# Performance work log

Hardware: AMD Instinct MI355X
Metric: run time of the kernel (lower is better)

## Reference

```python
import jax, jax.numpy as jnp
import numpy as np
import math

# Model dims (see shape_source)
N_EMBD = 2048
QK_H = 128      # per-head qk dim
V_H = 128       # per-head v dim
Q_DIM = N_EMBD                 # 2048 -> 16 query heads
N_HEAD = Q_DIM // QK_H         # 16
KV_HEAD = N_HEAD // 4          # 4 (GQA)
K_DIM = KV_HEAD * QK_H         # 512
V_DIM = KV_HEAD * V_H          # 512
D_KV = K_DIM + V_DIM           # 1024, S6 channel dim
D_STATE = 16                   # S6 state size
DT_RANK = math.ceil(D_KV / 16) # 'auto' -> 64
WINDOW = 512
B, T = 1, 4096


def setup_inputs() -> dict:
    key = jax.random.key(0)
    ks = jax.random.split(key, 8)
    x = jax.random.normal(ks[0], (B, T, N_EMBD), jnp.float32)
    W_attn = jax.random.normal(ks[1], (Q_DIM + K_DIM + V_DIM, N_EMBD), jnp.float32) * 0.02
    # S6 params (canonical Mamba S6 init: A = -exp(A_log), A_log = log(1..N))
    A_log = jnp.log(jnp.arange(1, D_STATE + 1, dtype=jnp.float32))[None, :] * jnp.ones((D_KV, 1), jnp.float32)
    x_proj_w = jax.random.normal(ks[2], (DT_RANK + 2 * D_STATE, D_KV), jnp.float32) * 0.02
    dt_proj_w = jax.random.normal(ks[3], (D_KV, DT_RANK), jnp.float32) * 0.02
    dt_proj_b = jax.random.normal(ks[4], (D_KV,), jnp.float32) * 0.1
    D_param = jnp.ones((D_KV,), jnp.float32)
    W_o = jax.random.normal(ks[5], (N_EMBD, Q_DIM), jnp.float32) * 0.02
    return dict(x=x, W_attn=W_attn, A_log=A_log, x_proj_w=x_proj_w,
                dt_proj_w=dt_proj_w, dt_proj_b=dt_proj_b, D_param=D_param,
                W_o=W_o, window_size=WINDOW)


def s6_scan(u, A_log, x_proj_w, dt_proj_w, dt_proj_b, D_param):
    """Canonical S6 selective scan. u: (B, T, D) -> (B, T, D)."""
    Bb, Tt, D = u.shape
    N = A_log.shape[1]
    dt_rank = dt_proj_w.shape[1]
    x_dbl = jnp.einsum('btd,ed->bte', u, x_proj_w)          # (B,T,dt_rank+2N)
    dt, Bm, Cm = jnp.split(x_dbl, [dt_rank, dt_rank + N], axis=-1)
    delta = jax.nn.softplus(jnp.einsum('btr,dr->btd', dt, dt_proj_w) + dt_proj_b)  # (B,T,D)
    A = -jnp.exp(A_log)                                      # (D,N), negative
    dA = jnp.exp(delta[..., None] * A)                       # (B,T,D,N)
    dBu = delta[..., None] * Bm[:, :, None, :] * u[..., None]  # (B,T,D,N)

    def step(h, inp):
        dA_t, dBu_t, C_t = inp
        h = dA_t * h + dBu_t                                 # (B,D,N)
        y = jnp.einsum('bdn,bn->bd', h, C_t)
        return h, y

    h0 = jnp.zeros((Bb, D, N), u.dtype)
    _, ys = jax.lax.scan(step, h0,
                         (dA.transpose(1, 0, 2, 3), dBu.transpose(1, 0, 2, 3), Cm.transpose(1, 0, 2)))
    y = ys.transpose(1, 0, 2)                                # (B,T,D)
    return y + D_param * u


def sliding_window_attn(q, k, v, window, scale):
    """Causal sliding-window attention; query i attends to j in [i-(window-1), i].
    q: (B,T,H,dh), k/v: (B,T,Hk,dh). Blockwise with one look-back block."""
    Bb, Tt, H, dh = q.shape
    Hk = k.shape[2]
    G = H // Hk
    k = jnp.repeat(k, G, axis=2)
    v = jnp.repeat(v, G, axis=2)
    W = window
    nb = Tt // W
    # (B,H,nb,W,dh)
    qb = q.reshape(Bb, nb, W, H, dh).transpose(0, 3, 1, 2, 4)
    kb = k.reshape(Bb, nb, W, H, dh).transpose(0, 3, 1, 2, 4)
    vb = v.reshape(Bb, nb, W, H, dh).transpose(0, 3, 1, 2, 4)
    # previous block (zeros for first block)
    kprev = jnp.pad(kb, ((0, 0), (0, 0), (1, 0), (0, 0), (0, 0)))[:, :, :nb]
    vprev = jnp.pad(vb, ((0, 0), (0, 0), (1, 0), (0, 0), (0, 0)))[:, :, :nb]
    k2 = jnp.concatenate([kprev, kb], axis=3)                # (B,H,nb,2W,dh)
    v2 = jnp.concatenate([vprev, vb], axis=3)
    scores = jnp.einsum('bhwid,bhwjd->bhwij', qb * scale, k2)  # (B,H,nb,W,2W)
    i = jnp.arange(W)[:, None]
    j = jnp.arange(2 * W)[None, :]
    rel = i + W - j                                          # absolute i - j
    base_mask = (rel >= 0) & (rel <= W - 1)                  # causal & within window
    blk = jnp.arange(nb)[:, None, None]
    valid = base_mask[None] & ((j[None] >= W) | (blk > 0))   # first block: no look-back
    neg = jnp.finfo(jnp.float32).max
    scores = jnp.where(valid[None, None], scores, -neg)
    attn = jax.nn.softmax(scores.astype(jnp.float32), axis=-1).astype(q.dtype)
    out = jnp.einsum('bhwij,bhwjd->bhwid', attn, v2)         # (B,H,nb,W,dh)
    return out.transpose(0, 2, 3, 1, 4).reshape(Bb, Tt, H, dh)


def reference(x, W_attn, A_log, x_proj_w, dt_proj_w, dt_proj_b, D_param, W_o, window_size):
    Bb, Tt, C = x.shape
    qkv = jnp.einsum('btc,oc->bto', x, W_attn)
    q = qkv[..., :Q_DIM]
    kv = qkv[..., Q_DIM:]
    kv = s6_scan(kv, A_log, x_proj_w, dt_proj_w, dt_proj_b, D_param)
    k = kv[..., :K_DIM]
    v = kv[..., K_DIM:]
    q = q.reshape(Bb, Tt, N_HEAD, QK_H)
    k = k.reshape(Bb, Tt, KV_HEAD, QK_H)
    v = v.reshape(Bb, Tt, KV_HEAD, V_H)
    scale = 1.0 / math.sqrt(QK_H)
    y = sliding_window_attn(q, k, v, window_size, scale)     # (B,T,H,v_h)
    y = y.reshape(Bb, Tt, -1)
    return jnp.einsum('bto,no->btn', y, W_o)
```

## Files before the change

kernel.cpp:

```cpp
#include <hip/hip_runtime.h>
#include <hip/hip_bf16.h>

typedef __hip_bfloat16 bf16;
typedef __attribute__((ext_vector_type(8))) short bf16x8;
typedef __attribute__((ext_vector_type(4))) float f32x4;

#define T_SEQ 4096
#define NEMBD 2048
#define QKVD  3072
#define QDIM  2048
#define DKV   1024
#define KDIM  512
#define NH    16
#define DH    128
#define NST   16
#define DTR   64
#define WIN   512
#define NCHUNK 64
#define CLEN   64

__device__ inline float bf2f(bf16 x) { return __bfloat162float(x); }

struct F8 { float v[8]; };

__device__ inline F8 load_b8(const bf16* p) {
  union { uint4 q; unsigned short s[8]; } u;
  u.q = *reinterpret_cast<const uint4*>(p);
  F8 r;
#pragma unroll
  for (int i = 0; i < 8; i++) r.v[i] = __uint_as_float((unsigned)u.s[i] << 16);
  return r;
}

__device__ inline F8 load8(const void* base, size_t idx, int f32flag) {
  if (f32flag) {
    const float4* p = reinterpret_cast<const float4*>((const float*)base + idx);
    float4 a = p[0], b = p[1];
    F8 r;
    r.v[0]=a.x; r.v[1]=a.y; r.v[2]=a.z; r.v[3]=a.w;
    r.v[4]=b.x; r.v[5]=b.y; r.v[6]=b.z; r.v[7]=b.w;
    return r;
  }
  return load_b8((const bf16*)base + idx);
}

__device__ inline float load1(const void* base, size_t idx, int f32flag) {
  return f32flag ? ((const float*)base)[idx] : bf2f(((const bf16*)base)[idx]);
}

__device__ inline unsigned short f2b_bits(float f) {
  bf16 h = __float2bfloat16(f);
  union { bf16 h; unsigned short u; } c; c.h = h; return c.u;
}

__device__ inline ushort4 pack4(float a, float b, float c, float d) {
  ushort4 r; r.x = f2b_bits(a); r.y = f2b_bits(b); r.z = f2b_bits(c); r.w = f2b_bits(d);
  return r;
}

__device__ inline void gld_lds16(const void* g, void* l) {
  __builtin_amdgcn_global_load_lds(
      (const __attribute__((address_space(1))) unsigned int*)g,
      (__attribute__((address_space(3))) unsigned int*)l, 16, 0, 0);
}

__global__ void detect_dtype(const unsigned short* __restrict__ x, int* __restrict__ flag) {
  if (threadIdx.x == 0 && blockIdx.x == 0) {
    int c = 0;
    for (int i = 0; i < 128; i++) {
      float v = __uint_as_float((unsigned)x[i] << 16);
      float a = fabsf(v);
      if (a >= 1e-8f && a <= 1e4f) c++;
    }
    flag[0] = (c >= 120) ? 0 : 1;
  }
}

__global__ __launch_bounds__(256) void cvt_bf16(
    const void* __restrict__ in, const int* __restrict__ dflag,
    unsigned short* __restrict__ out, int n8)
{
  int i = blockIdx.x * 256 + threadIdx.x;
  if (i >= n8) return;
  const int f = dflag[0];
  F8 v = load8(in, (size_t)i * 8, f);
  ushort4* o = (ushort4*)(out + (size_t)i * 8);
  o[0] = pack4(v.v[0], v.v[1], v.v[2], v.v[3]);
  o[1] = pack4(v.v[4], v.v[5], v.v[6], v.v[7]);
}

__global__ __launch_bounds__(512, 2) void gemm_wide(
    const unsigned short* __restrict__ A, const unsigned short* __restrict__ B,
    int M, int N, int K, int mode,
    bf16* __restrict__ oq, bf16* __restrict__ ou, float* __restrict__ oc)
{
  __shared__ unsigned short lds[2][384 * 64];
  const int tid = threadIdx.x;
  const int wave = tid >> 6, lane = tid & 63;
  const int quad = lane >> 4, l16 = lane & 15;
  const int wm = wave >> 1, wn = wave & 1;
  const int nbx = N >> 7;
  const int nwg = gridDim.x;
  const int chunk = nwg >> 3;
  const int swz = (blockIdx.x & 7) * chunk + (blockIdx.x >> 3);
  const int bm = (swz / nbx) * 256, bn = (swz % nbx) * 128;

  const int lrow = lane >> 3;
  const int lslot = (lane & 7) ^ lrow;
  const unsigned short* Abase = A + (size_t)(bm + wave * 8 + lrow) * K + lslot * 8;
  const unsigned short* Bbase = B + (size_t)(bn + wave * 8 + lrow) * K + lslot * 8;

  const int x7 = l16 & 7;
  const int s0 = ((0 + quad) ^ x7) * 8;
  const int s1 = ((4 + quad) ^ x7) * 8;
  const int arow0 = (wm * 64 + l16) * 64;
  const int brow0 = (256 + wn * 64 + l16) * 64;

  f32x4 acc[4][4];
#pragma unroll
  for (int i = 0; i < 4; i++)
#pragma unroll
    for (int j = 0; j < 4; j++) acc[i][j] = f32x4{0.f, 0.f, 0.f, 0.f};

  const int NT = K >> 6;

#pragma unroll
  for (int grp = 0; grp < 4; grp++)
    gld_lds16(Abase + (size_t)grp * 64 * K, &lds[0][(grp * 64 + wave * 8) * 64]);
#pragma unroll
  for (int grp = 0; grp < 2; grp++)
    gld_lds16(Bbase + (size_t)grp * 64 * K, &lds[0][(256 + grp * 64 + wave * 8) * 64]);
#pragma unroll
  for (int grp = 0; grp < 4; grp++)
    gld_lds16(Abase + (size_t)grp * 64 * K + 64, &lds[1][(grp * 64 + wave * 8) * 64]);
#pragma unroll
  for (int grp = 0; grp < 2; grp++)
    gld_lds16(Bbase + (size_t)grp * 64 * K + 64, &lds[1][(256 + grp * 64 + wave * 8) * 64]);
  asm volatile("s_waitcnt vmcnt(6)" ::: "memory");
  __builtin_amdgcn_sched_barrier(0);
  __builtin_amdgcn_s_barrier();

#define MM(m, n) \
  acc[m][n] = __builtin_amdgcn_mfma_f32_16x16x32_bf16(aF[m][0], bF[n][0], acc[m][n], 0, 0, 0); \
  acc[m][n] = __builtin_amdgcn_mfma_f32_16x16x32_bf16(aF[m][1], bF[n][1], acc[m][n], 0, 0, 0);

  for (int g = 0; g < NT; ++g) {
    const unsigned short* L = lds[g & 1];
    unsigned short* Lw = (unsigned short*)L;
    const bool stF = (g + 2) < NT;
    const size_t kF = (size_t)(g + 2) * 64;

    bf16x8 aF[4][2], bF[4][2];

#pragma unroll
    for (int m = 0; m < 4; m++) {
      aF[m][0] = *(const bf16x8*)&L[arow0 + m * 1024 + s0];
      aF[m][1] = *(const bf16x8*)&L[arow0 + m * 1024 + s1];
    }
    bF[0][0] = *(const bf16x8*)&L[brow0 +    0 + s0];
    bF[0][1] = *(const bf16x8*)&L[brow0 +    0 + s1];
    bF[1][0] = *(const bf16x8*)&L[brow0 + 1024 + s0];
    bF[1][1] = *(const bf16x8*)&L[brow0 + 1024 + s1];
    __builtin_amdgcn_s_barrier();
    if (stF) {
#pragma unroll
      for (int grp = 0; grp < 4; grp++)
        gld_lds16(Abase + (size_t)grp * 64 * K + kF, &Lw[(grp * 64 + wave * 8) * 64]);
    }
    __builtin_amdgcn_s_setprio(1);
    MM(0,0); MM(0,1); MM(1,0); MM(1,1);
    MM(2,0); MM(2,1); MM(3,0); MM(3,1);
    __builtin_amdgcn_s_setprio(0);
    __builtin_amdgcn_s_barrier();

    bF[2][0] = *(const bf16x8*)&L[brow0 + 2048 + s0];
    bF[2][1] = *(const bf16x8*)&L[brow0 + 2048 + s1];
    bF[3][0] = *(const bf16x8*)&L[brow0 + 3072 + s0];
    bF[3][1] = *(const bf16x8*)&L[brow0 + 3072 + s1];
    __builtin_amdgcn_s_barrier();
    if (stF) {
#pragma unroll
      for (int grp = 0; grp < 2; grp++)
        gld_lds16(Bbase + (size_t)grp * 64 * K + kF, &Lw[(256 + grp * 64 + wave * 8) * 64]);
    }
    __builtin_amdgcn_s_setprio(1);
    MM(0,2); MM(0,3); MM(1,2); MM(1,3);
    MM(2,2); MM(2,3); MM(3,2); MM(3,3);
    __builtin_amdgcn_s_setprio(0);
    if (stF) { asm volatile("s_waitcnt vmcnt(6)" ::: "memory"); }
    else     { asm volatile("s_waitcnt vmcnt(0)" ::: "memory"); }
    __builtin_amdgcn_sched_barrier(0);
    __builtin_amdgcn_s_barrier();
  }
#undef MM

#pragma unroll
  for (int m = 0; m < 4; m++)
#pragma unroll
    for (int n = 0; n < 4; n++) {
      int gm0 = bm + wm * 64 + m * 16 + quad * 4;
      int gn  = bn + wn * 64 + n * 16 + l16;
#pragma unroll
      for (int r = 0; r < 4; r++) {
        int gm = gm0 + r;
        float v = acc[m][n][r];
        if (mode == 0) {
          if (gn < QDIM) oq[(size_t)gm * QDIM + gn] = __float2bfloat16(v);
          else           ou[(size_t)gm * DKV + (gn - QDIM)] = __float2bfloat16(v);
        } else {
          oc[(size_t)gm * N + gn] = v;
        }
      }
    }
}

__global__ __launch_bounds__(256) void xdbl_mfma(
    const bf16* __restrict__ u, const unsigned short* __restrict__ xpw_bf,
    float* __restrict__ xd)
{
  __shared__ unsigned short Us[64 * 32];
  __shared__ unsigned short Ws[96 * 32];
  const int tid = threadIdx.x;
  const int wave = tid >> 6, lane = tid & 63;
  const int quad = lane >> 4, l16 = lane & 15;
  const int t0 = blockIdx.x * 64;
  const unsigned short* ub = (const unsigned short*)u;

  f32x4 acc[6];
#pragma unroll
  for (int j = 0; j < 6; j++) acc[j] = f32x4{0.f, 0.f, 0.f, 0.f};

  const int urow = tid >> 2, ucol = (tid & 3) * 8;
  const int wrow0 = tid >> 2, wcol0 = (tid & 3) * 8;
  const int wrow1 = (256 + tid) >> 2;

  uint4 upre = *(const uint4*)(ub + (size_t)(t0 + urow) * DKV + ucol);
  uint4 wpre0 = *(const uint4*)(xpw_bf + (size_t)wrow0 * DKV + wcol0);
  uint4 wpre1 = (tid < 128) ? *(const uint4*)(xpw_bf + (size_t)wrow1 * DKV + wcol0)
                            : uint4{0, 0, 0, 0};

  for (int k0 = 0; k0 < DKV; k0 += 32) {
    __syncthreads();
    *(uint4*)&Us[urow * 32 + ucol] = upre;
    *(uint4*)&Ws[wrow0 * 32 + wcol0] = wpre0;
    if (tid < 128) *(uint4*)&Ws[wrow1 * 32 + wcol0] = wpre1;
    __syncthreads();

    int kn = (k0 + 32 < DKV) ? (k0 + 32) : k0;
    upre  = *(const uint4*)(ub + (size_t)(t0 + urow) * DKV + kn + ucol);
    wpre0 = *(const uint4*)(xpw_bf + (size_t)wrow0 * DKV + kn + wcol0);
    if (tid < 128) wpre1 = *(const uint4*)(xpw_bf + (size_t)wrow1 * DKV + kn + wcol0);

    bf16x8 a = *(const bf16x8*)&Us[(wave * 16 + l16) * 32 + quad * 8];
#pragma unroll
    for (int j = 0; j < 6; j++) {
      bf16x8 b = *(const bf16x8*)&Ws[(j * 16 + l16) * 32 + quad * 8];
      acc[j] = __builtin_amdgcn_mfma_f32_16x16x32_bf16(a, b, acc[j], 0, 0, 0);
    }
  }

#pragma unroll
  for (int j = 0; j < 6; j++)
#pragma unroll
    for (int r = 0; r < 4; r++) {
      int t = t0 + wave * 16 + quad * 4 + r;
      xd[(size_t)t * 96 + j * 16 + l16] = acc[j][r];
    }
}

__global__ __launch_bounds__(256) void delta_mfma(
    const float* __restrict__ xd, const unsigned short* __restrict__ dtw_bf,
    const void* __restrict__ dtb, const int* __restrict__ dflag,
    bf16* __restrict__ delta)
{
  __shared__ unsigned short Xs[64 * 72];
  __shared__ unsigned short Ws[128 * 72];
  const int tid = threadIdx.x;
  const int wave = tid >> 6, lane = tid & 63;
  const int quad = lane >> 4, l16 = lane & 15;
  const int t0 = blockIdx.y * 64, d0 = blockIdx.x * 128;

  for (int e = tid; e < 64 * 8; e += 256) {
    int row = e >> 3, c8 = (e & 7) * 8;
    const float* p = xd + (size_t)(t0 + row) * 96 + c8;
    float4 a = *(const float4*)p, b = *(const float4*)(p + 4);
    *(ushort4*)&Xs[row * 72 + c8]     = pack4(a.x, a.y, a.z, a.w);
    *(ushort4*)&Xs[row * 72 + c8 + 4] = pack4(b.x, b.y, b.z, b.w);
  }
  for (int e = tid; e < 128 * 8; e += 256) {
    int row = e >> 3, c8 = (e & 7) * 8;
    *(uint4*)&Ws[row * 72 + c8] = *(const uint4*)(dtw_bf + (size_t)(d0 + row) * DTR + c8);
  }
  __syncthreads();

  bf16x8 a0 = *(const bf16x8*)&Xs[(wave * 16 + l16) * 72 + quad * 8];
  bf16x8 a1 = *(const bf16x8*)&Xs[(wave * 16 + l16) * 72 + 32 + quad * 8];

  f32x4 acc[8];
#pragma unroll
  for (int j = 0; j < 8; j++) {
    bf16x8 b0 = *(const bf16x8*)&Ws[(j * 16 + l16) * 72 + quad * 8];
    bf16x8 b1 = *(const bf16x8*)&Ws[(j * 16 + l16) * 72 + 32 + quad * 8];
    acc[j] = __builtin_amdgcn_mfma_f32_16x16x32_bf16(a0, b0, f32x4{0.f, 0.f, 0.f, 0.f}, 0, 0, 0);
    acc[j] = __builtin_amdgcn_mfma_f32_16x16x32_bf16(a1, b1, acc[j], 0, 0, 0);
  }

  const int f = dflag[0];
#pragma unroll
  for (int j = 0; j < 8; j++) {
    int d = d0 + j * 16 + l16;
    float bias = load1(dtb, d, f);
#pragma unroll
    for (int r = 0; r < 4; r++) {
      int t = t0 + wave * 16 + quad * 4 + r;
      float v = acc[j][r] + bias;
      float sp = fmaxf(v, 0.f) + log1pf(expf(-fabsf(v)));
      delta[(size_t)t * DKV + d] = __float2bfloat16(sp);
    }
  }
}

__global__ __launch_bounds__(256) void scan_pass1(
    const bf16* __restrict__ delta, const bf16* __restrict__ u,
    const float* __restrict__ xd, const void* __restrict__ A_log,
    const int* __restrict__ dflag, float* __restrict__ Pb, float* __restrict__ Hl)
{
  const int gid = blockIdx.x * 256 + threadIdx.x;
  const int c = gid >> 14;
  const int r = gid & 16383;
  const int d = r >> 4, n = r & 15;
  const int f = dflag[0];
  const float A = -expf(load1(A_log, d * NST + n, f));
  float p = 1.f, h = 0.f;
  const int t0 = c * CLEN;
  for (int tt = 0; tt < CLEN; tt++) {
    int t = t0 + tt;
    float dl = bf2f(delta[(size_t)t * DKV + d]);
    float uu = bf2f(u[(size_t)t * DKV + d]);
    float bm = xd[(size_t)t * 96 + DTR + n];
    float a = expf(dl * A);
    h = a * h + dl * bm * uu;
    p *= a;
  }
  Pb[gid] = p;
  Hl[gid] = h;
}

__global__ __launch_bounds__(256) void scan_combine(
    float* __restrict__ Pb, const float* __restrict__ Hl)
{
  const int idx = blockIdx.x * 256 + threadIdx.x;
  float run = 0.f;
  for (int c = 0; c < NCHUNK; c++) {
    size_t off = (size_t)c * 16384 + idx;
    float p = Pb[off], hl = Hl[off];
    Pb[off] = run;
    run = p * run + hl;
  }
}

__global__ __launch_bounds__(256) void scan_pass2(
    const bf16* __restrict__ delta, bf16* __restrict__ u,
    const float* __restrict__ xd, const void* __restrict__ A_log,
    const void* __restrict__ Dp, const int* __restrict__ dflag,
    const float* __restrict__ Hin)
{
  const int gid = blockIdx.x * 256 + threadIdx.x;
  const int c = gid >> 14;
  const int r = gid & 16383;
  const int d = r >> 4, n = r & 15;
  const int f = dflag[0];
  const float A = -expf(load1(A_log, d * NST + n, f));
  const float dpar = load1(Dp, d, f);
  float h = Hin[gid];
  const int t0 = c * CLEN;
  for (int tt = 0; tt < CLEN; tt++) {
    int t = t0 + tt;
    float dl = bf2f(delta[(size_t)t * DKV + d]);
    float uu = bf2f(u[(size_t)t * DKV + d]);
    float bm = xd[(size_t)t * 96 + DTR + n];
    float cm = xd[(size_t)t * 96 + DTR + NST + n];
    float a = expf(dl * A);
    h = a * h + dl * bm * uu;
    float part = h * cm;
    part += __shfl_xor(part, 1);
    part += __shfl_xor(part, 2);
    part += __shfl_xor(part, 4);
    part += __shfl_xor(part, 8);
    if (n == 0) u[(size_t)t * DKV + d] = __float2bfloat16(part + dpar * uu);
  }
}

__global__ __launch_bounds__(256) void vtrans(
    const bf16* __restrict__ kv, unsigned short* __restrict__ vt)
{
  __shared__ float tile[64][68];
  const int tt0 = blockIdx.x * 64, d0 = blockIdx.y * 64;
  const int tid = threadIdx.x;
  for (int e = tid; e < 64 * 8; e += 256) {
    int row = e >> 3, c8 = (e & 7) * 8;
    F8 v = load_b8(kv + (size_t)(tt0 + row) * DKV + KDIM + d0 + c8);
#pragma unroll
    for (int j = 0; j < 8; j++) tile[row][c8 + j] = v.v[j];
  }
  __syncthreads();
  for (int e = tid; e < 64 * 8; e += 256) {
    int dd = e >> 3, t8 = (e & 7) * 8;
    float vv[8];
#pragma unroll
    for (int j = 0; j < 8; j++) vv[j] = tile[t8 + j][dd];
    ushort4* o = (ushort4*)(vt + (size_t)(d0 + dd) * T_SEQ + tt0 + t8);
    o[0] = pack4(vv[0], vv[1], vv[2], vv[3]);
    o[1] = pack4(vv[4], vv[5], vv[6], vv[7]);
  }
}

__global__ __launch_bounds__(256, 4) void attn_mfma(
    const bf16* __restrict__ q, const bf16* __restrict__ kv,
    const unsigned short* __restrict__ vt, bf16* __restrict__ y)
{
  __shared__ unsigned short Ks[32 * 136];
  __shared__ unsigned short Vts[128 * 40];
  __shared__ unsigned short Ps[4][16 * 40];
  const int tid = threadIdx.x;
  const int wave = tid >> 6, lane = tid & 63;
  const int quad = lane >> 4, l16 = lane & 15;
  const int qt = blockIdx.x, h = blockIdx.y, kvh = h >> 2;
  const int t0 = qt * 64;
  const float scale = 0.088388347648318447f;

  bf16x8 af[4];
#pragma unroll
  for (int s = 0; s < 4; s++)
    af[s] = *(const bf16x8*)(q + (size_t)(t0 + wave * 16 + l16) * QDIM
                             + h * DH + s * 32 + quad * 8);

  const int krow = tid >> 4, kc8 = (tid & 15) * 8;
  const int vrow = tid >> 2, vc8 = (tid & 3) * 8;
  const bf16* kgp = kv + (size_t)kvh * DH;
  const unsigned short* vgp = vt + (size_t)(kvh * DH) * T_SEQ;

  float m_r[4], l_p[4];
  f32x4 O[8];
#pragma unroll
  for (int r = 0; r < 4; r++) { m_r[r] = -1e30f; l_p[r] = 0.f; }
#pragma unroll
  for (int dt = 0; dt < 8; dt++) O[dt] = f32x4{0.f, 0.f, 0.f, 0.f};

  const int kb_start = (t0 > WIN - 1) ? ((t0 - (WIN - 1)) >> 5) : 0;
  const int kb_end = (t0 + 63) >> 5;

  uint4 kp0, kp1, vp0, vp1;
  {
    const int kb = kb_start;
    kp0 = *(const uint4*)(kgp + (size_t)(kb * 32 + krow) * DKV + kc8);
    kp1 = *(const uint4*)(kgp + (size_t)(kb * 32 + 16 + krow) * DKV + kc8);
    vp0 = *(const uint4*)(vgp + (size_t)vrow * T_SEQ + kb * 32 + vc8);
    vp1 = *(const uint4*)(vgp + (size_t)(vrow + 64) * T_SEQ + kb * 32 + vc8);
  }

  for (int kb = kb_start; kb <= kb_end; kb++) {
    __syncthreads();
    *(uint4*)&Ks[krow * 136 + kc8]        = kp0;
    *(uint4*)&Ks[(krow + 16) * 136 + kc8] = kp1;
    *(uint4*)&Vts[vrow * 40 + vc8]        = vp0;
    *(uint4*)&Vts[(vrow + 64) * 40 + vc8] = vp1;
    __syncthreads();

    if (kb < kb_end) {
      const int kn = kb + 1;
      kp0 = *(const uint4*)(kgp + (size_t)(kn * 32 + krow) * DKV + kc8);
      kp1 = *(const uint4*)(kgp + (size_t)(kn * 32 + 16 + krow) * DKV + kc8);
      vp0 = *(const uint4*)(vgp + (size_t)vrow * T_SEQ + kn * 32 + vc8);
      vp1 = *(const uint4*)(vgp + (size_t)(vrow + 64) * T_SEQ + kn * 32 + vc8);
    }

    f32x4 S0 = f32x4{0.f, 0.f, 0.f, 0.f}, S1 = f32x4{0.f, 0.f, 0.f, 0.f};
#pragma unroll
    for (int s = 0; s < 4; s++) {
      bf16x8 b0 = *(const bf16x8*)&Ks[(l16) * 136 + s * 32 + quad * 8];
      bf16x8 b1 = *(const bf16x8*)&Ks[(16 + l16) * 136 + s * 32 + quad * 8];
      S0 = __builtin_amdgcn_mfma_f32_16x16x32_bf16(af[s], b0, S0, 0, 0, 0);
      S1 = __builtin_amdgcn_mfma_f32_16x16x32_bf16(af[s], b1, S1, 0, 0, 0);
    }

    const int ka0 = kb * 32 + l16;
    const int ka1 = ka0 + 16;
    const bool full = (kb * 32 >= t0 + 63 - (WIN - 1)) && (kb * 32 + 31 <= t0);

    float v0r[4], v1r[4];
    bool x0r[4], x1r[4];
    bool ok = true;
#pragma unroll
    for (int r = 0; r < 4; r++) {
      int qa = t0 + wave * 16 + quad * 4 + r;
      float v0 = S0[r] * scale, v1 = S1[r] * scale;
      bool x0 = true, x1 = true;
      if (!full) {
        x0 = (ka0 <= qa) && (ka0 > qa - WIN);
        x1 = (ka1 <= qa) && (ka1 > qa - WIN);
        if (!x0) v0 = -1e30f;
        if (!x1) v1 = -1e30f;
      }
      v0r[r] = v0; v1r[r] = v1; x0r[r] = x0; x1r[r] = x1;
      ok = ok && (fmaxf(v0, v1) <= m_r[r] + 8.f);
    }

    if (!__all((int)ok)) {
#pragma unroll
      for (int r = 0; r < 4; r++) {
        float rm = fmaxf(v0r[r], v1r[r]);
        rm = fmaxf(rm, __shfl_xor(rm, 1));
        rm = fmaxf(rm, __shfl_xor(rm, 2));
        rm = fmaxf(rm, __shfl_xor(rm, 4));
        rm = fmaxf(rm, __shfl_xor(rm, 8));
        float mnew = fmaxf(m_r[r], rm);
        float al = __expf(m_r[r] - mnew);
        m_r[r] = mnew;
        l_p[r] *= al;
#pragma unroll
        for (int dt = 0; dt < 8; dt++) O[dt][r] *= al;
      }
    }

#pragma unroll
    for (int r = 0; r < 4; r++) {
      float p0 = x0r[r] ? __expf(v0r[r] - m_r[r]) : 0.f;
      float p1 = x1r[r] ? __expf(v1r[r] - m_r[r]) : 0.f;
      l_p[r] += p0 + p1;
      Ps[wave][(quad * 4 + r) * 40 + l16]      = f2b_bits(p0);
      Ps[wave][(quad * 4 + r) * 40 + 16 + l16] = f2b_bits(p1);
    }

    bf16x8 pa = *(const bf16x8*)&Ps[wave][l16 * 40 + quad * 8];
#pragma unroll
    for (int dt = 0; dt < 8; dt++) {
      bf16x8 b = *(const bf16x8*)&Vts[(dt * 16 + l16) * 40 + quad * 8];
      O[dt] = __builtin_amdgcn_mfma_f32_16x16x32_bf16(pa, b, O[dt], 0, 0, 0);
    }
  }

  float inv[4];
#pragma unroll
  for (int r = 0; r < 4; r++) {
    float l = l_p[r];
    l += __shfl_xor(l, 1);
    l += __shfl_xor(l, 2);
    l += __shfl_xor(l, 4);
    l += __shfl_xor(l, 8);
    inv[r] = 1.f / l;
  }
#pragma unroll
  for (int dt = 0; dt < 8; dt++)
#pragma unroll
    for (int r = 0; r < 4; r++) {
      int row = t0 + wave * 16 + quad * 4 + r;
      y[(size_t)row * QDIM + h * DH + dt * 16 + l16] = __float2bfloat16(O[dt][r] * inv[r]);
    }
}

extern "C" void kernel_launch(void* const* d_in, const int* in_sizes, int n_in,
                              void* d_out, int out_size, void* d_ws, size_t ws_size,
                              hipStream_t stream)
{
  const void* x      = d_in[0];
  const void* W_attn = d_in[1];
  const void* A_log  = d_in[2];
  const void* xpw    = d_in[3];
  const void* dtw    = d_in[4];
  const void* dtb    = d_in[5];
  const void* Dp     = d_in[6];
  const void* W_o    = d_in[7];

  char* ws = (char*)d_ws;
  int*   dflag = (int*)ws;   ws += 256;
  bf16*  u     = (bf16*)ws;  ws += (size_t)T_SEQ * DKV * 2;
  float* xd    = (float*)ws; ws += (size_t)T_SEQ * 96 * 4;
  char*  yreg  = ws;
  bf16*  delta = (bf16*)ws;  ws += (size_t)T_SEQ * DKV * 2;
  float* Pb    = (float*)ws; ws += (size_t)NCHUNK * DKV * NST * 4;
  float* Hl    = (float*)ws; ws += (size_t)NCHUNK * DKV * NST * 4;
  unsigned short* x_bf  = (unsigned short*)ws; ws += (size_t)T_SEQ * NEMBD * 2;
  unsigned short* wa_bf = (unsigned short*)ws; ws += (size_t)QKVD * NEMBD * 2;
  unsigned short* wo_bf = (unsigned short*)ws; ws += (size_t)NEMBD * QDIM * 2;
  unsigned short* vt    = (unsigned short*)ws; ws += (size_t)KDIM * T_SEQ * 2;
  unsigned short* xpw_bf = (unsigned short*)ws; ws += (size_t)96 * DKV * 2;
  unsigned short* dtw_bf = (unsigned short*)ws; ws += (size_t)DKV * DTR * 2;
  bf16*  y     = (bf16*)yreg;

  bf16*  q_bf = (bf16*)d_out;
  float* out  = (float*)d_out;

  detect_dtype<<<1, 64, 0, stream>>>((const unsigned short*)x, dflag);
  cvt_bf16<<<(T_SEQ * NEMBD / 8 + 255) / 256, 256, 0, stream>>>(x, dflag, x_bf, T_SEQ * NEMBD / 8);
  cvt_bf16<<<(QKVD * NEMBD / 8 + 255) / 256, 256, 0, stream>>>(W_attn, dflag, wa_bf, QKVD * NEMBD / 8);
  cvt_bf16<<<(NEMBD * QDIM / 8 + 255) / 256, 256, 0, stream>>>(W_o, dflag, wo_bf, NEMBD * QDIM / 8);
  cvt_bf16<<<(96 * DKV / 8 + 255) / 256, 256, 0, stream>>>(xpw, dflag, xpw_bf, 96 * DKV / 8);
  cvt_bf16<<<(DKV * DTR / 8 + 255) / 256, 256, 0, stream>>>(dtw, dflag, dtw_bf, DKV * DTR / 8);

  gemm_wide<<<(T_SEQ / 256) * (QKVD / 128), 512, 0, stream>>>(
      x_bf, wa_bf, T_SEQ, QKVD, NEMBD, 0, q_bf, u, nullptr);
  xdbl_mfma<<<T_SEQ / 64, 256, 0, stream>>>(u, xpw_bf, xd);
  delta_mfma<<<dim3(DKV / 128, T_SEQ / 64), 256, 0, stream>>>(xd, dtw_bf, dtb, dflag, delta);
  scan_pass1<<<4096, 256, 0, stream>>>(delta, u, xd, A_log, dflag, Pb, Hl);
  scan_combine<<<64, 256, 0, stream>>>(Pb, Hl);
  scan_pass2<<<4096, 256, 0, stream>>>(delta, u, xd, A_log, Dp, dflag, Pb);
  vtrans<<<dim3(T_SEQ / 64, KDIM / 64), 256, 0, stream>>>(u, vt);
  attn_mfma<<<dim3(T_SEQ / 64, NH), 256, 0, stream>>>(q_bf, u, vt, y);
  gemm_wide<<<(T_SEQ / 256) * (QDIM / 128), 512, 0, stream>>>(
      (const unsigned short*)y, wo_bf, T_SEQ, QDIM, QDIM, 1, nullptr, nullptr, out);
}
```

Before: 438.3 us.

## Enlarge GEMM block tile to 256x256 with 2x4 wave layout

The wide bf16 GEMM's block tile grows from 256x128 to 256x256. Each of the 8 waves now computes a 128x64 sub-tile with 32 accumulators. Global-to-LDS staging and the MFMA sequence are rescheduled into four interleaved phases per k-step, and both GEMM launches get half as many blocks. The goal is more operand reuse per LDS load and less global traffic per FLOP. The cost is double the LDS (128KB per block, which likely allows only one block per CU) and fewer blocks than CUs for both GEMMs, so part of the GPU may sit idle.

```diff
diff --git a/kernel.cpp b/kernel.cpp
--- a/kernel.cpp
+++ b/kernel.cpp
@@ -94,61 +94,64 @@
     int M, int N, int K, int mode,
     bf16* __restrict__ oq, bf16* __restrict__ ou, float* __restrict__ oc)
 {
-  __shared__ unsigned short lds[2][384 * 64];
+  __shared__ unsigned short lds[2][512 * 64];
   const int tid = threadIdx.x;
   const int wave = tid >> 6, lane = tid & 63;
   const int quad = lane >> 4, l16 = lane & 15;
-  const int wm = wave >> 1, wn = wave & 1;
-  const int nbx = N >> 7;
+  const int wm = wave >> 2, wn = wave & 3;
+  const int nbx = N >> 8;
   const int nwg = gridDim.x;
   const int chunk = nwg >> 3;
   const int swz = (blockIdx.x & 7) * chunk + (blockIdx.x >> 3);
-  const int bm = (swz / nbx) * 256, bn = (swz % nbx) * 128;
+  const int bm = (swz / nbx) * 256, bn = (swz % nbx) * 256;
 
   const int lrow = lane >> 3;
   const int lslot = (lane & 7) ^ lrow;
-  const unsigned short* Abase = A + (size_t)(bm + wave * 8 + lrow) * K + lslot * 8;
-  const unsigned short* Bbase = B + (size_t)(bn + wave * 8 + lrow) * K + lslot * 8;
+  const int arow_st = (wave & 3) * 16 + (wave >> 2) * 128;
+  const int brow_st = (wave >> 1) * 64 + (wave & 1) * 16;
+  const unsigned short* AbaseS = A + (size_t)(bm + arow_st + lrow) * K + lslot * 8;
+  const unsigned short* BbaseS = B + (size_t)(bn + brow_st + lrow) * K + lslot * 8;
+
+#define ST_A(b, h, kt) \
+  gld_lds16(AbaseS + (size_t)((h) * 64) * K + (size_t)(kt) * 64, \
+            &lds[b][(arow_st + (h) * 64) * 64]); \
+  gld_lds16(AbaseS + (size_t)((h) * 64 + 8) * K + (size_t)(kt) * 64, \
+            &lds[b][(arow_st + (h) * 64 + 8) * 64]);
+#define ST_B(b, h, kt) \
+  gld_lds16(BbaseS + (size_t)((h) * 32) * K + (size_t)(kt) * 64, \
+            &lds[b][(256 + brow_st + (h) * 32) * 64]); \
+  gld_lds16(BbaseS + (size_t)((h) * 32 + 8) * K + (size_t)(kt) * 64, \
+            &lds[b][(256 + brow_st + (h) * 32 + 8) * 64]);
 
   const int x7 = l16 & 7;
   const int s0 = ((0 + quad) ^ x7) * 8;
   const int s1 = ((4 + quad) ^ x7) * 8;
-  const int arow0 = (wm * 64 + l16) * 64;
+  const int arow0 = (wm * 128 + l16) * 64;
   const int brow0 = (256 + wn * 64 + l16) * 64;
 
-  f32x4 acc[4][4];
-#pragma unroll
-  for (int i = 0; i < 4; i++)
+  f32x4 acc[8][4];
+#pragma unroll
+  for (int i = 0; i < 8; i++)
 #pragma unroll
     for (int j = 0; j < 4; j++) acc[i][j] = f32x4{0.f, 0.f, 0.f, 0.f};
 
   const int NT = K >> 6;
 
-#pragma unroll
-  for (int grp = 0; grp < 4; grp++)
-    gld_lds16(Abase + (size_t)grp * 64 * K, &lds[0][(grp * 64 + wave * 8) * 64]);
-#pragma unroll
-  for (int grp = 0; grp < 2; grp++)
-    gld_lds16(Bbase + (size_t)grp * 64 * K, &lds[0][(256 + grp * 64 + wave * 8) * 64]);
-#pragma unroll
-  for (int grp = 0; grp < 4; grp++)
-    gld_lds16(Abase + (size_t)grp * 64 * K + 64, &lds[1][(grp * 64 + wave * 8) * 64]);
-#pragma unroll
-  for (int grp = 0; grp < 2; grp++)
-    gld_lds16(Bbase + (size_t)grp * 64 * K + 64, &lds[1][(256 + grp * 64 + wave * 8) * 64]);
-  asm volatile("s_waitcnt vmcnt(6)" ::: "memory");
+  ST_A(0, 0, 0); ST_A(0, 1, 0); ST_B(0, 0, 0); ST_B(0, 1, 0);
+  ST_A(1, 0, 1); ST_A(1, 1, 1); ST_B(1, 0, 1); ST_B(1, 1, 1);
+  asm volatile("s_waitcnt vmcnt(8)" ::: "memory");
   __builtin_amdgcn_sched_barrier(0);
   __builtin_amdgcn_s_barrier();
 
-#define MM(m, n) \
-  acc[m][n] = __builtin_amdgcn_mfma_f32_16x16x32_bf16(aF[m][0], bF[n][0], acc[m][n], 0, 0, 0); \
-  acc[m][n] = __builtin_amdgcn_mfma_f32_16x16x32_bf16(aF[m][1], bF[n][1], acc[m][n], 0, 0, 0);
+#define MM(i, j, am, bn_) \
+  acc[i][j] = __builtin_amdgcn_mfma_f32_16x16x32_bf16(aF[am][0], bF[bn_][0], acc[i][j], 0, 0, 0); \
+  acc[i][j] = __builtin_amdgcn_mfma_f32_16x16x32_bf16(aF[am][1], bF[bn_][1], acc[i][j], 0, 0, 0);
 
   for (int g = 0; g < NT; ++g) {
     const unsigned short* L = lds[g & 1];
-    unsigned short* Lw = (unsigned short*)L;
+    const int sb = g & 1;
     const bool stF = (g + 2) < NT;
-    const size_t kF = (size_t)(g + 2) * 64;
+    const int kt2 = g + 2;
 
     bf16x8 aF[4][2], bF[4][2];
 
@@ -157,53 +160,69 @@
       aF[m][0] = *(const bf16x8*)&L[arow0 + m * 1024 + s0];
       aF[m][1] = *(const bf16x8*)&L[arow0 + m * 1024 + s1];
     }
-    bF[0][0] = *(const bf16x8*)&L[brow0 +    0 + s0];
-    bF[0][1] = *(const bf16x8*)&L[brow0 +    0 + s1];
-    bF[1][0] = *(const bf16x8*)&L[brow0 + 1024 + s0];
-    bF[1][1] = *(const bf16x8*)&L[brow0 + 1024 + s1];
-    __builtin_amdgcn_s_barrier();
-    if (stF) {
-#pragma unroll
-      for (int grp = 0; grp < 4; grp++)
-        gld_lds16(Abase + (size_t)grp * 64 * K + kF, &Lw[(grp * 64 + wave * 8) * 64]);
-    }
+#pragma unroll
+    for (int n = 0; n < 2; n++) {
+      bF[n][0] = *(const bf16x8*)&L[brow0 + n * 1024 + s0];
+      bF[n][1] = *(const bf16x8*)&L[brow0 + n * 1024 + s1];
+    }
+    __builtin_amdgcn_s_barrier();
     __builtin_amdgcn_s_setprio(1);
-    MM(0,0); MM(0,1); MM(1,0); MM(1,1);
-    MM(2,0); MM(2,1); MM(3,0); MM(3,1);
+    MM(0,0,0,0); MM(0,1,0,1); MM(1,0,1,0); MM(1,1,1,1);
+    MM(2,0,2,0); MM(2,1,2,1); MM(3,0,3,0); MM(3,1,3,1);
     __builtin_amdgcn_s_setprio(0);
     __builtin_amdgcn_s_barrier();
 
-    bF[2][0] = *(const bf16x8*)&L[brow0 + 2048 + s0];
-    bF[2][1] = *(const bf16x8*)&L[brow0 + 2048 + s1];
-    bF[3][0] = *(const bf16x8*)&L[brow0 + 3072 + s0];
-    bF[3][1] = *(const bf16x8*)&L[brow0 + 3072 + s1];
-    __builtin_amdgcn_s_barrier();
-    if (stF) {
-#pragma unroll
-      for (int grp = 0; grp < 2; grp++)
-        gld_lds16(Bbase + (size_t)grp * 64 * K + kF, &Lw[(256 + grp * 64 + wave * 8) * 64]);
-    }
+#pragma unroll
+    for (int n = 0; n < 2; n++) {
+      bF[2 + n][0] = *(const bf16x8*)&L[brow0 + 2048 + n * 1024 + s0];
+      bF[2 + n][1] = *(const bf16x8*)&L[brow0 + 2048 + n * 1024 + s1];
+    }
+    if (stF) { ST_A(sb, 0, kt2); }
+    __builtin_amdgcn_s_barrier();
     __builtin_amdgcn_s_setprio(1);
-    MM(0,2); MM(0,3); MM(1,2); MM(1,3);
-    MM(2,2); MM(2,3); MM(3,2); MM(3,3);
+    MM(0,2,0,2); MM(0,3,0,3); MM(1,2,1,2); MM(1,3,1,3);
+    MM(2,2,2,2); MM(2,3,2,3); MM(3,2,3,2); MM(3,3,3,3);
     __builtin_amdgcn_s_setprio(0);
-    if (stF) { asm volatile("s_waitcnt vmcnt(6)" ::: "memory"); }
+    __builtin_amdgcn_s_barrier();
+
+#pragma unroll
+    for (int m = 0; m < 4; m++) {
+      aF[m][0] = *(const bf16x8*)&L[arow0 + 4096 + m * 1024 + s0];
+      aF[m][1] = *(const bf16x8*)&L[arow0 + 4096 + m * 1024 + s1];
+    }
+    if (stF) { ST_B(sb, 0, kt2); ST_B(sb, 1, kt2); }
+    __builtin_amdgcn_s_barrier();
+    __builtin_amdgcn_s_setprio(1);
+    MM(4,2,0,2); MM(4,3,0,3); MM(5,2,1,2); MM(5,3,1,3);
+    MM(6,2,2,2); MM(6,3,2,3); MM(7,2,3,2); MM(7,3,3,3);
+    __builtin_amdgcn_s_setprio(0);
+    __builtin_amdgcn_s_barrier();
+
+    if (stF) { ST_A(sb, 1, kt2); }
+    __builtin_amdgcn_s_barrier();
+    __builtin_amdgcn_s_setprio(1);
+    MM(4,0,0,0); MM(4,1,0,1); MM(5,0,1,0); MM(5,1,1,1);
+    MM(6,0,2,0); MM(6,1,2,1); MM(7,0,3,0); MM(7,1,3,1);
+    __builtin_amdgcn_s_setprio(0);
+    if (stF) { asm volatile("s_waitcnt vmcnt(8)" ::: "memory"); }
     else     { asm volatile("s_waitcnt vmcnt(0)" ::: "memory"); }
     __builtin_amdgcn_sched_barrier(0);
     __builtin_amdgcn_s_barrier();
   }
 #undef MM
-
-#pragma unroll
-  for (int m = 0; m < 4; m++)
-#pragma unroll
-    for (int n = 0; n < 4; n++) {
-      int gm0 = bm + wm * 64 + m * 16 + quad * 4;
-      int gn  = bn + wn * 64 + n * 16 + l16;
+#undef ST_A
+#undef ST_B
+
+#pragma unroll
+  for (int i = 0; i < 8; i++)
+#pragma unroll
+    for (int j = 0; j < 4; j++) {
+      int gm0 = bm + wm * 128 + i * 16 + quad * 4;
+      int gn  = bn + wn * 64 + j * 16 + l16;
 #pragma unroll
       for (int r = 0; r < 4; r++) {
         int gm = gm0 + r;
-        float v = acc[m][n][r];
+        float v = acc[i][j][r];
         if (mode == 0) {
           if (gn < QDIM) oq[(size_t)gm * QDIM + gn] = __float2bfloat16(v);
           else           ou[(size_t)gm * DKV + (gn - QDIM)] = __float2bfloat16(v);
@@ -598,7 +617,7 @@
   cvt_bf16<<<(96 * DKV / 8 + 255) / 256, 256, 0, stream>>>(xpw, dflag, xpw_bf, 96 * DKV / 8);
   cvt_bf16<<<(DKV * DTR / 8 + 255) / 256, 256, 0, stream>>>(dtw, dflag, dtw_bf, DKV * DTR / 8);
 
-  gemm_wide<<<(T_SEQ / 256) * (QKVD / 128), 512, 0, stream>>>(
+  gemm_wide<<<(T_SEQ / 256) * (QKVD / 256), 512, 0, stream>>>(
       x_bf, wa_bf, T_SEQ, QKVD, NEMBD, 0, q_bf, u, nullptr);
   xdbl_mfma<<<T_SEQ / 64, 256, 0, stream>>>(u, xpw_bf, xd);
   delta_mfma<<<dim3(DKV / 128, T_SEQ / 64), 256, 0, stream>>>(xd, dtw_bf, dtb, dflag, delta);
@@ -607,6 +626,6 @@
   scan_pass2<<<4096, 256, 0, stream>>>(delta, u, xd, A_log, Dp, dflag, Pb);
   vtrans<<<dim3(T_SEQ / 64, KDIM / 64), 256, 0, stream>>>(u, vt);
   attn_mfma<<<dim3(T_SEQ / 64, NH), 256, 0, stream>>>(q_bf, u, vt, y);
-  gemm_wide<<<(T_SEQ / 256) * (QDIM / 128), 512, 0, stream>>>(
+  gemm_wide<<<(T_SEQ / 256) * (QDIM / 256), 512, 0, stream>>>(
       (const unsigned short*)y, wo_bf, T_SEQ, QDIM, QDIM, 1, nullptr, nullptr, out);
 }
```

Result: no change. 441.3 us (+0.7%).
